# Optimization experiments

Hardware: AMD Instinct MI355X
Metric: run time of the kernel (lower is better)

The kernel has to match this reference:

```python
import jax, jax.numpy as jnp
import numpy as np


def setup_inputs() -> dict:
    key = jax.random.key(0)
    k1, k2 = jax.random.split(key)
    Hf, Wf, C, N = 512, 1024, 128, 400
    feat_map = jax.random.normal(k1, (1, C, Hf, Wf), dtype=jnp.float32)
    seg_small = jax.random.randint(k2, (Hf, Wf), 0, N, dtype=jnp.int32)
    return {"feat_map": feat_map, "seg_small": seg_small, "num_segments": N}


def reference(feat_map, seg_small, num_segments):
    # Faithful vectorized form of StereoGraphNet.aggregate_node_features:
    # per-superpixel masked mean of CNN features, zeros for empty segments.
    fmap = feat_map[0]                               # [C, Hf, Wf]
    C = fmap.shape[0]
    seg = seg_small.reshape(-1)                      # [P] segment id per pixel
    vals = fmap.reshape(C, -1).T                     # [P, C] pixel features
    sums = jax.ops.segment_sum(vals, seg, num_segments=num_segments)  # [N, C]
    counts = jax.ops.segment_sum(
        jnp.ones(seg.shape, dtype=vals.dtype), seg, num_segments=num_segments
    )                                                # [N]
    means = sums / jnp.maximum(counts, 1.0)[:, None]
    # empty segments -> zero feature (torch.zeros(C) branch in original)
    node_feats = jnp.where(counts[:, None] > 0, means, jnp.zeros((), vals.dtype))
    return node_feats                                # [N, C]
```

## Files before the change

kernel.cpp:

```cpp
#include <hip/hip_runtime.h>


#define NSEG_MAX 512
#define C_FAST   128
#define C2       (C_FAST / 2)
#define PXW      128
#define LROW     67
#define HB       512
#define NB_MAX   1024

__device__ __forceinline__ unsigned pk_bf16(float lo, float hi)
{
    unsigned a = __builtin_bit_cast(unsigned, lo);
    unsigned b = __builtin_bit_cast(unsigned, hi);
    a += 0x7FFFu + ((a >> 16) & 1u);
    b += 0x7FFFu + ((b >> 16) & 1u);
    return (a >> 16) | (b & 0xFFFF0000u);
}


__global__ __launch_bounds__(128)
void s0_hist(const int* __restrict__ seg, int* __restrict__ pr,
             int* __restrict__ hist)
{
    __shared__ int h[NSEG_MAX];
    const int t = threadIdx.x, b = blockIdx.x;
    for (int i = t; i < NSEG_MAX; i += 128) h[i] = 0;
    __syncthreads();
    const long p0 = (long)b * HB;
    const int4 s4 = *(const int4*)(seg + p0 + t * 4);
    const int r0 = atomicAdd(&h[s4.x], 1);
    const int r1 = atomicAdd(&h[s4.y], 1);
    const int r2 = atomicAdd(&h[s4.z], 1);
    const int r3 = atomicAdd(&h[s4.w], 1);
    int4 pk;
    pk.x = (r0 << 9) | s4.x;  pk.y = (r1 << 9) | s4.y;
    pk.z = (r2 << 9) | s4.z;  pk.w = (r3 << 9) | s4.w;
    *(int4*)(pr + p0 + t * 4) = pk;
    __syncthreads();
    for (int i = t; i < NSEG_MAX; i += 128)
        hist[i * NB_MAX + b] = h[i];
}

__global__ __launch_bounds__(1024)
void s1_scanb(int* __restrict__ hist, int* __restrict__ cnt, int NB)
{
    __shared__ int a[NB_MAX];
    const int s = blockIdx.x, t = threadIdx.x;
    const int v = (t < NB) ? hist[s * NB_MAX + t] : 0;
    a[t] = v;
    __syncthreads();
    for (int off = 1; off < NB_MAX; off <<= 1) {
        const int x = (t >= off) ? a[t - off] : 0;
        __syncthreads();
        a[t] += x;
        __syncthreads();
    }
    if (t < NB) hist[s * NB_MAX + t] = a[t] - v;
    if (t == NB_MAX - 1) cnt[s] = a[t];
}

__global__ __launch_bounds__(NSEG_MAX)
void s2_scans(const int* __restrict__ cnt, int* __restrict__ offs)
{
    __shared__ int a[NSEG_MAX];
    const int t = threadIdx.x;
    const int v = cnt[t];
    a[t] = v;
    __syncthreads();
    for (int off = 1; off < NSEG_MAX; off <<= 1) {
        const int x = (t >= off) ? a[t - off] : 0;
        __syncthreads();
        a[t] += x;
        __syncthreads();
    }
    offs[t] = a[t] - v;
    if (t == NSEG_MAX - 1) offs[NSEG_MAX] = a[t];
}

__global__ __launch_bounds__(256)
void s3_scatter(const float* __restrict__ feat, const int* __restrict__ pr,
                const int* __restrict__ hist, const int* __restrict__ offs,
                unsigned* __restrict__ fs, long P)
{
    __shared__ unsigned tile[PXW * LROW];
    __shared__ int srank[PXW];

    const int tid = threadIdx.x;
    const long p0 = (long)blockIdx.x * PXW;
    const int bh = blockIdx.x >> 2;

    if (tid < PXW) {
        const int v = pr[p0 + tid];
        const int s = v & (NSEG_MAX - 1);
        srank[tid] = offs[s] + hist[s * NB_MAX + bh] + (v >> 9);
    }

    const int l = tid & 31, r = tid >> 5;
    #pragma unroll
    for (int it = 0; it < 8; ++it) {
        const int c2 = it * 8 + r;
        const float* f0 = feat + (long)(2 * c2) * P + p0 + l * 4;
        const float4 va = *(const float4*)(f0);
        const float4 vb = *(const float4*)(f0 + P);
        unsigned* tr = tile + c2;
        const int pxb = 4 * l;
        tr[(pxb + 0) * LROW] = pk_bf16(va.x, vb.x);
        tr[(pxb + 1) * LROW] = pk_bf16(va.y, vb.y);
        tr[(pxb + 2) * LROW] = pk_bf16(va.z, vb.z);
        tr[(pxb + 3) * LROW] = pk_bf16(va.w, vb.w);
    }
    __syncthreads();

    const int wave = tid >> 6, wl = tid & 63;
    for (int px = wave; px < PXW; px += 4) {
        const unsigned u = tile[px * LROW + wl];
        fs[(long)srank[px] * C2 + wl] = u;
    }
}

__global__ __launch_bounds__(256)
void s4_zero(float* __restrict__ p, int n)
{
    const int i = blockIdx.x * 256 + threadIdx.x;
    if (i < n) p[i] = 0.f;
}

__global__ __launch_bounds__(256)
void s5_reduce(const unsigned* __restrict__ fs, const int* __restrict__ offs,
               float* __restrict__ out)
{
    __shared__ int so[NSEG_MAX + 1];
    const int tid = threadIdx.x;
    for (int i = tid; i <= NSEG_MAX; i += 256) so[i] = offs[i];
    __syncthreads();

    const int l = tid & 63;
    const int r0 = blockIdx.x * 256 + (tid >> 6) * 64;

    int lo = 0, hi = NSEG_MAX;
    while (lo < hi) {
        const int mid = (lo + hi + 1) >> 1;
        if (so[mid] <= r0) lo = mid; else hi = mid - 1;
    }
    int s = lo;

    float a0 = 0.f, a1 = 0.f;
    const unsigned* bp = fs + (long)r0 * C2 + l;
    #pragma unroll 1
    for (int g = 0; g < 8; ++g) {
        unsigned u[8];
        #pragma unroll
        for (int k = 0; k < 8; ++k) u[k] = bp[(long)(g * 8 + k) * C2];
        #pragma unroll
        for (int k = 0; k < 8; ++k) {
            const int rr = r0 + g * 8 + k;
            if (rr >= so[s + 1]) {
                unsafeAtomicAdd(&out[s * C_FAST + 2 * l],     a0);
                unsafeAtomicAdd(&out[s * C_FAST + 2 * l + 1], a1);
                a0 = a1 = 0.f;
                do { ++s; } while (rr >= so[s + 1]);
            }
            a0 += __builtin_bit_cast(float, u[k] << 16);
            a1 += __builtin_bit_cast(float, u[k] & 0xFFFF0000u);
        }
    }
    unsafeAtomicAdd(&out[s * C_FAST + 2 * l],     a0);
    unsafeAtomicAdd(&out[s * C_FAST + 2 * l + 1], a1);
}

__global__ __launch_bounds__(256)
void s6_final(float* __restrict__ out, const int* __restrict__ cnt, int nc)
{
    const int t = blockIdx.x * 256 + threadIdx.x;
    if (t >= nc) return;
    const int n = cnt[t >> 7];
    const float v = out[t];
    out[t] = (n > 0) ? v / (float)n : 0.f;
}


__global__ __launch_bounds__(512)
void k0_zero(int* __restrict__ cnt, int n)
{
    const int t = threadIdx.x;
    if (t < n) cnt[t] = 0;
}

__global__ __launch_bounds__(256)
void k1_hist(const int* __restrict__ seg, int* __restrict__ cnt, int N)
{
    __shared__ int h[NSEG_MAX];
    const int t = threadIdx.x;
    for (int i = t; i < N; i += 256) h[i] = 0;
    __syncthreads();
    const long base = (long)blockIdx.x * 1024 + t * 4;
    const int4 s4 = *(const int4*)(seg + base);
    atomicAdd(&h[s4.x], 1); atomicAdd(&h[s4.y], 1);
    atomicAdd(&h[s4.z], 1); atomicAdd(&h[s4.w], 1);
    __syncthreads();
    for (int i = t; i < N; i += 256)
        if (h[i]) atomicAdd(&cnt[i], h[i]);
}

__global__ __launch_bounds__(NSEG_MAX)
void k2_scan(const int* __restrict__ cnt, int* __restrict__ offs,
             int* __restrict__ cursor, int N)
{
    __shared__ int a[NSEG_MAX];
    const int t = threadIdx.x;
    const int v = (t < N) ? cnt[t] : 0;
    a[t] = v;
    __syncthreads();
    for (int off = 1; off < NSEG_MAX; off <<= 1) {
        const int x = (t >= off) ? a[t - off] : 0;
        __syncthreads();
        a[t] += x;
        __syncthreads();
    }
    if (t < N) { const int e = a[t] - v; offs[t] = e; cursor[t] = e; }
}

__global__ __launch_bounds__(256)
void k3_scatter(const float* __restrict__ feat, const int* __restrict__ seg,
                int* __restrict__ cursor, unsigned* __restrict__ fs, long P)
{
    __shared__ unsigned tile[PXW * LROW];
    __shared__ int srank[PXW];
    const int tid = threadIdx.x;
    const long p0 = (long)blockIdx.x * PXW;
    const int l = tid & 31, r = tid >> 5;
    #pragma unroll
    for (int it = 0; it < 8; ++it) {
        const int c2 = it * 8 + r;
        const float* f0 = feat + (long)(2 * c2) * P + p0 + l * 4;
        const float4 va = *(const float4*)(f0);
        const float4 vb = *(const float4*)(f0 + P);
        unsigned* tr = tile + c2;
        const int pxb = 4 * l;
        tr[(pxb + 0) * LROW] = pk_bf16(va.x, vb.x);
        tr[(pxb + 1) * LROW] = pk_bf16(va.y, vb.y);
        tr[(pxb + 2) * LROW] = pk_bf16(va.z, vb.z);
        tr[(pxb + 3) * LROW] = pk_bf16(va.w, vb.w);
    }
    if (tid < PXW) {
        const int s = seg[p0 + tid];
        srank[tid] = atomicAdd(&cursor[s], 1);
    }
    __syncthreads();
    const int wave = tid >> 6, wl = tid & 63;
    for (int px = wave; px < PXW; px += 4) {
        const unsigned u = tile[px * LROW + wl];
        fs[(long)srank[px] * C2 + wl] = u;
    }
}

__global__ __launch_bounds__(512)
void k4_reduce(const unsigned* __restrict__ fs, const int* __restrict__ offs,
               const int* __restrict__ cnt, float* __restrict__ out)
{
    __shared__ float red[8][C_FAST];
    const int s = blockIdx.x;
    const int tid = threadIdx.x, l = tid & 63, j = tid >> 6;
    const int start = offs[s], n = cnt[s];
    float a0 = 0.f, a1 = 0.f;
    const unsigned* base = fs + (long)start * C2 + l;
    for (int i = j; i < n; i += 8) {
        const unsigned u = base[(long)i * C2];
        a0 += __builtin_bit_cast(float, u << 16);
        a1 += __builtin_bit_cast(float, u & 0xFFFF0000u);
    }
    red[j][2 * l]     = a0;
    red[j][2 * l + 1] = a1;
    __syncthreads();
    if (tid < C_FAST) {
        float sum = 0.f;
        #pragma unroll
        for (int q = 0; q < 8; ++q) sum += red[q][tid];
        out[(long)s * C_FAST + tid] = (n > 0) ? sum / (float)n : 0.f;
    }
}


#define FB_THREADS 256
#define FB_CPB 2

__global__ __launch_bounds__(256)
void fb_zero(float* __restrict__ p, int n)
{
    const int i = blockIdx.x * 256 + threadIdx.x;
    if (i < n) p[i] = 0.f;
}

__global__ __launch_bounds__(FB_THREADS, 4)
void fb_partial(const float* __restrict__ feat, const int* __restrict__ seg,
                float* __restrict__ acc, float* __restrict__ cnt,
                long P, int N, int kIters)
{
    __shared__ float s_sum[FB_CPB][NSEG_MAX];
    __shared__ int   s_cnt[NSEG_MAX];
    const int tid = threadIdx.x;
    const int g = blockIdx.x, w = blockIdx.y;
    const int c0 = g * FB_CPB;
    const bool doCnt = (g == 0);
    for (int i = tid; i < FB_CPB * NSEG_MAX; i += FB_THREADS) (&s_sum[0][0])[i] = 0.f;
    for (int i = tid; i < NSEG_MAX; i += FB_THREADS) s_cnt[i] = 0;
    __syncthreads();
    const long pbase = (long)w * kIters * (FB_THREADS * 4);
    const int*   sp  = seg + pbase + (long)tid * 4;
    const float* fp0 = feat + (long)c0 * P + pbase + (long)tid * 4;
    const float* fp1 = fp0 + P;
    for (int k = 0; k < kIters; ++k) {
        const long off = (long)k * (FB_THREADS * 4);
        const int4 s4 = *(const int4*)(sp + off);
        const float4 a = *(const float4*)(fp0 + off);
        const float4 b = *(const float4*)(fp1 + off);
        unsafeAtomicAdd(&s_sum[0][s4.x], a.x);
        unsafeAtomicAdd(&s_sum[0][s4.y], a.y);
        unsafeAtomicAdd(&s_sum[0][s4.z], a.z);
        unsafeAtomicAdd(&s_sum[0][s4.w], a.w);
        unsafeAtomicAdd(&s_sum[1][s4.x], b.x);
        unsafeAtomicAdd(&s_sum[1][s4.y], b.y);
        unsafeAtomicAdd(&s_sum[1][s4.z], b.z);
        unsafeAtomicAdd(&s_sum[1][s4.w], b.w);
        if (doCnt) {
            atomicAdd(&s_cnt[s4.x], 1); atomicAdd(&s_cnt[s4.y], 1);
            atomicAdd(&s_cnt[s4.z], 1); atomicAdd(&s_cnt[s4.w], 1);
        }
    }
    __syncthreads();
    for (int i = tid; i < FB_CPB * N; i += FB_THREADS) {
        const int dc = i / N, s = i - dc * N;
        unsafeAtomicAdd(&acc[(long)(c0 + dc) * N + s], s_sum[dc][s]);
    }
    if (doCnt)
        for (int s = tid; s < N; s += FB_THREADS)
            unsafeAtomicAdd(&cnt[s], (float)s_cnt[s]);
}

__global__ __launch_bounds__(256)
void fb_finalize(const float* __restrict__ acc, const float* __restrict__ cnt,
                 float* __restrict__ out, int N, int C)
{
    const int t = blockIdx.x * 256 + threadIdx.x;
    if (t >= N * C) return;
    const int s = t / C, c = t - s * C;
    const float ct = cnt[s];
    out[t] = (ct > 0.f) ? acc[(long)c * N + s] / ct : 0.f;
}


extern "C" void kernel_launch(void* const* d_in, const int* in_sizes, int n_in,
                              void* d_out, int out_size, void* d_ws, size_t ws_size,
                              hipStream_t stream)
{
    const float* feat = (const float*)d_in[0];
    const int*   seg  = (const int*)d_in[1];
    float*       out  = (float*)d_out;

    const long P = in_sizes[1];
    const int  C = (int)(in_sizes[0] / P);
    const int  N = out_size / C;

    const int NB = (int)(P / HB);
    const size_t need_new = (size_t)P * C2 * 4 + (size_t)P * 4 +
                            (size_t)NSEG_MAX * NB_MAX * 4 +
                            (size_t)(2 * NSEG_MAX + 1) * 4;
    const size_t need_old = (size_t)P * C2 * 4 + 3u * NSEG_MAX * 4;

    const bool shapeOK = (C == C_FAST) && (N <= NSEG_MAX);
    const bool fastNew = shapeOK && (P % HB == 0) && (NB <= NB_MAX) &&
                         (P % 256 == 0) && ws_size >= need_new;
    const bool fastOld = shapeOK && (P % PXW == 0) && (P % 1024 == 0) &&
                         ws_size >= need_old;

    if (fastNew) {
        unsigned* fs = (unsigned*)d_ws;
        int* pr   = (int*)(fs + (size_t)P * C2);
        int* hist = pr + P;
        int* cnt  = hist + (size_t)NSEG_MAX * NB_MAX;
        int* offs = cnt + NSEG_MAX;
        const int nc = N * C_FAST;

        s0_hist  <<<NB, 128, 0, stream>>>(seg, pr, hist);
        s1_scanb <<<NSEG_MAX, 1024, 0, stream>>>(hist, cnt, NB);
        s2_scans <<<1, NSEG_MAX, 0, stream>>>(cnt, offs);
        s4_zero  <<<(nc + 255) / 256, 256, 0, stream>>>(out, nc);
        s3_scatter<<<(int)(P / PXW), 256, 0, stream>>>(feat, pr, hist, offs, fs, P);
        s5_reduce<<<(int)(P / 256), 256, 0, stream>>>(fs, offs, out);
        s6_final <<<(nc + 255) / 256, 256, 0, stream>>>(out, cnt, nc);
    } else if (fastOld) {
        unsigned* fs  = (unsigned*)d_ws;
        int* cnt    = (int*)(fs + (size_t)P * C2);
        int* offs   = cnt + NSEG_MAX;
        int* cursor = offs + NSEG_MAX;

        k0_zero  <<<1, 512, 0, stream>>>(cnt, N);
        k1_hist  <<<(int)(P / 1024), 256, 0, stream>>>(seg, cnt, N);
        k2_scan  <<<1, NSEG_MAX, 0, stream>>>(cnt, offs, cursor, N);
        k3_scatter<<<(int)(P / PXW), 256, 0, stream>>>(feat, seg, cursor, fs, P);
        k4_reduce<<<N, 512, 0, stream>>>(fs, offs, cnt, out);
    } else {
        int W = 32;
        while (W > 1 && (P % ((long)W * FB_THREADS * 4)) != 0) W >>= 1;
        const int kIters = (int)(P / ((long)W * FB_THREADS * 4));
        float* acc = (float*)d_ws;
        float* cnt = acc + (size_t)C * N;
        const int nz = C * N + N;
        fb_zero<<<(nz + 255) / 256, 256, 0, stream>>>(acc, nz);
        fb_partial<<<dim3(C / FB_CPB, W), dim3(FB_THREADS), 0, stream>>>(
            feat, seg, acc, cnt, P, N, kIters);
        fb_finalize<<<(N * C + 255) / 256, 256, 0, stream>>>(acc, cnt, out, N, C);
    }
}
```

Measured before the change: 421.1 us.

## Replace atomic segmented reduce with per-segment block reduce and enlarge histogram blocks

The fast path now reduces with one 512-thread block per segment that reads that segment's contiguous sorted rows. This replaces the row-partitioned reduce that flushed partial sums with float atomics. It also drops the separate zero and finalize kernels, so the pipeline launches two fewer kernels. The histogram block size doubles (with twice the threads) and the scatter kernel goes to 512 threads, which halves the per-block histogram table. The risk is uneven per-segment work and fewer loads in flight per thread in the reduce.

```diff
diff --git a/kernel.cpp b/kernel.cpp
--- a/kernel.cpp
+++ b/kernel.cpp
@@ -6,8 +6,8 @@
 #define C2       (C_FAST / 2)
 #define PXW      128
 #define LROW     67
-#define HB       512
-#define NB_MAX   1024
+#define HB       1024
+#define NB_MAX   512
 
 __device__ __forceinline__ unsigned pk_bf16(float lo, float hi)
 {
@@ -19,13 +19,13 @@
 }
 
 
-__global__ __launch_bounds__(128)
+__global__ __launch_bounds__(256)
 void s0_hist(const int* __restrict__ seg, int* __restrict__ pr,
              int* __restrict__ hist)
 {
     __shared__ int h[NSEG_MAX];
     const int t = threadIdx.x, b = blockIdx.x;
-    for (int i = t; i < NSEG_MAX; i += 128) h[i] = 0;
+    for (int i = t; i < NSEG_MAX; i += 256) h[i] = 0;
     __syncthreads();
     const long p0 = (long)b * HB;
     const int4 s4 = *(const int4*)(seg + p0 + t * 4);
@@ -38,11 +38,11 @@
     pk.z = (r2 << 9) | s4.z;  pk.w = (r3 << 9) | s4.w;
     *(int4*)(pr + p0 + t * 4) = pk;
     __syncthreads();
-    for (int i = t; i < NSEG_MAX; i += 128)
+    for (int i = t; i < NSEG_MAX; i += 256)
         hist[i * NB_MAX + b] = h[i];
 }
 
-__global__ __launch_bounds__(1024)
+__global__ __launch_bounds__(NB_MAX)
 void s1_scanb(int* __restrict__ hist, int* __restrict__ cnt, int NB)
 {
     __shared__ int a[NB_MAX];
@@ -78,7 +78,7 @@
     if (t == NSEG_MAX - 1) offs[NSEG_MAX] = a[t];
 }
 
-__global__ __launch_bounds__(256)
+__global__ __launch_bounds__(512)
 void s3_scatter(const float* __restrict__ feat, const int* __restrict__ pr,
                 const int* __restrict__ hist, const int* __restrict__ offs,
                 unsigned* __restrict__ fs, long P)
@@ -88,7 +88,7 @@
 
     const int tid = threadIdx.x;
     const long p0 = (long)blockIdx.x * PXW;
-    const int bh = blockIdx.x >> 2;
+    const int bh = blockIdx.x >> 3;
 
     if (tid < PXW) {
         const int v = pr[p0 + tid];
@@ -96,10 +96,10 @@
         srank[tid] = offs[s] + hist[s * NB_MAX + bh] + (v >> 9);
     }
 
-    const int l = tid & 31, r = tid >> 5;
+    const int l = tid & 31, rr = tid >> 5;
     #pragma unroll
-    for (int it = 0; it < 8; ++it) {
-        const int c2 = it * 8 + r;
+    for (int it = 0; it < 4; ++it) {
+        const int c2 = it * 16 + rr;
         const float* f0 = feat + (long)(2 * c2) * P + p0 + l * 4;
         const float4 va = *(const float4*)(f0);
         const float4 vb = *(const float4*)(f0 + P);
@@ -113,70 +113,37 @@
     __syncthreads();
 
     const int wave = tid >> 6, wl = tid & 63;
-    for (int px = wave; px < PXW; px += 4) {
+    for (int px = wave; px < PXW; px += 8) {
         const unsigned u = tile[px * LROW + wl];
         fs[(long)srank[px] * C2 + wl] = u;
     }
 }
 
-__global__ __launch_bounds__(256)
-void s4_zero(float* __restrict__ p, int n)
-{
-    const int i = blockIdx.x * 256 + threadIdx.x;
-    if (i < n) p[i] = 0.f;
-}
-
-__global__ __launch_bounds__(256)
-void s5_reduce(const unsigned* __restrict__ fs, const int* __restrict__ offs,
-               float* __restrict__ out)
-{
-    __shared__ int so[NSEG_MAX + 1];
-    const int tid = threadIdx.x;
-    for (int i = tid; i <= NSEG_MAX; i += 256) so[i] = offs[i];
-    __syncthreads();
-
-    const int l = tid & 63;
-    const int r0 = blockIdx.x * 256 + (tid >> 6) * 64;
-
-    int lo = 0, hi = NSEG_MAX;
-    while (lo < hi) {
-        const int mid = (lo + hi + 1) >> 1;
-        if (so[mid] <= r0) lo = mid; else hi = mid - 1;
-    }
-    int s = lo;
+__global__ __launch_bounds__(512)
+void k4_reduce(const unsigned* __restrict__ fs, const int* __restrict__ offs,
+               const int* __restrict__ cnt, float* __restrict__ out)
+{
+    __shared__ float red[8][C_FAST];
+    const int s = blockIdx.x;
+    const int tid = threadIdx.x, l = tid & 63, j = tid >> 6;
+    const int start = offs[s], n = cnt[s];
 
     float a0 = 0.f, a1 = 0.f;
-    const unsigned* bp = fs + (long)r0 * C2 + l;
-    #pragma unroll 1
-    for (int g = 0; g < 8; ++g) {
-        unsigned u[8];
+    const unsigned* base = fs + (long)start * C2 + l;
+    for (int i = j; i < n; i += 8) {
+        const unsigned u = base[(long)i * C2];
+        a0 += __builtin_bit_cast(float, u << 16);
+        a1 += __builtin_bit_cast(float, u & 0xFFFF0000u);
+    }
+    red[j][2 * l]     = a0;
+    red[j][2 * l + 1] = a1;
+    __syncthreads();
+    if (tid < C_FAST) {
+        float sum = 0.f;
         #pragma unroll
-        for (int k = 0; k < 8; ++k) u[k] = bp[(long)(g * 8 + k) * C2];
-        #pragma unroll
-        for (int k = 0; k < 8; ++k) {
-            const int rr = r0 + g * 8 + k;
-            if (rr >= so[s + 1]) {
-                unsafeAtomicAdd(&out[s * C_FAST + 2 * l],     a0);
-                unsafeAtomicAdd(&out[s * C_FAST + 2 * l + 1], a1);
-                a0 = a1 = 0.f;
-                do { ++s; } while (rr >= so[s + 1]);
-            }
-            a0 += __builtin_bit_cast(float, u[k] << 16);
-            a1 += __builtin_bit_cast(float, u[k] & 0xFFFF0000u);
-        }
-    }
-    unsafeAtomicAdd(&out[s * C_FAST + 2 * l],     a0);
-    unsafeAtomicAdd(&out[s * C_FAST + 2 * l + 1], a1);
-}
-
-__global__ __launch_bounds__(256)
-void s6_final(float* __restrict__ out, const int* __restrict__ cnt, int nc)
-{
-    const int t = blockIdx.x * 256 + threadIdx.x;
-    if (t >= nc) return;
-    const int n = cnt[t >> 7];
-    const float v = out[t];
-    out[t] = (n > 0) ? v / (float)n : 0.f;
+        for (int q = 0; q < 8; ++q) sum += red[q][tid];
+        out[(long)s * C_FAST + tid] = (n > 0) ? sum / (float)n : 0.f;
+    }
 }
 
 
@@ -252,32 +219,6 @@
     for (int px = wave; px < PXW; px += 4) {
         const unsigned u = tile[px * LROW + wl];
         fs[(long)srank[px] * C2 + wl] = u;
-    }
-}
-
-__global__ __launch_bounds__(512)
-void k4_reduce(const unsigned* __restrict__ fs, const int* __restrict__ offs,
-               const int* __restrict__ cnt, float* __restrict__ out)
-{
-    __shared__ float red[8][C_FAST];
-    const int s = blockIdx.x;
-    const int tid = threadIdx.x, l = tid & 63, j = tid >> 6;
-    const int start = offs[s], n = cnt[s];
-    float a0 = 0.f, a1 = 0.f;
-    const unsigned* base = fs + (long)start * C2 + l;
-    for (int i = j; i < n; i += 8) {
-        const unsigned u = base[(long)i * C2];
-        a0 += __builtin_bit_cast(float, u << 16);
-        a1 += __builtin_bit_cast(float, u & 0xFFFF0000u);
-    }
-    red[j][2 * l]     = a0;
-    red[j][2 * l + 1] = a1;
-    __syncthreads();
-    if (tid < C_FAST) {
-        float sum = 0.f;
-        #pragma unroll
-        for (int q = 0; q < 8; ++q) sum += red[q][tid];
-        out[(long)s * C_FAST + tid] = (n > 0) ? sum / (float)n : 0.f;
     }
 }
 
@@ -370,7 +311,7 @@
 
     const bool shapeOK = (C == C_FAST) && (N <= NSEG_MAX);
     const bool fastNew = shapeOK && (P % HB == 0) && (NB <= NB_MAX) &&
-                         (P % 256 == 0) && ws_size >= need_new;
+                         ws_size >= need_new;
     const bool fastOld = shapeOK && (P % PXW == 0) && (P % 1024 == 0) &&
                          ws_size >= need_old;
 
@@ -380,15 +321,12 @@
         int* hist = pr + P;
         int* cnt  = hist + (size_t)NSEG_MAX * NB_MAX;
         int* offs = cnt + NSEG_MAX;
-        const int nc = N * C_FAST;
-
-        s0_hist  <<<NB, 128, 0, stream>>>(seg, pr, hist);
-        s1_scanb <<<NSEG_MAX, 1024, 0, stream>>>(hist, cnt, NB);
+
+        s0_hist  <<<NB, 256, 0, stream>>>(seg, pr, hist);
+        s1_scanb <<<NSEG_MAX, NB_MAX, 0, stream>>>(hist, cnt, NB);
         s2_scans <<<1, NSEG_MAX, 0, stream>>>(cnt, offs);
-        s4_zero  <<<(nc + 255) / 256, 256, 0, stream>>>(out, nc);
-        s3_scatter<<<(int)(P / PXW), 256, 0, stream>>>(feat, pr, hist, offs, fs, P);
-        s5_reduce<<<(int)(P / 256), 256, 0, stream>>>(fs, offs, out);
-        s6_final <<<(nc + 255) / 256, 256, 0, stream>>>(out, cnt, nc);
+        s3_scatter<<<(int)(P / PXW), 512, 0, stream>>>(feat, pr, hist, offs, fs, P);
+        k4_reduce<<<N, 512, 0, stream>>>(fs, offs, cnt, out);
     } else if (fastOld) {
         unsigned* fs  = (unsigned*)d_ws;
         int* cnt    = (int*)(fs + (size_t)P * C2);
```

Measured after the change: 470.8 us. +11.8%, slower.
